# Kernel optimization log

Measured on AMD Instinct MI355X. Metric: run time of the kernel, lower is better.

Reference implementation:

```python
import jax, jax.numpy as jnp
import numpy as np
import math

V, D, H, L, T, B = 32000, 768, 12, 4, 1024, 2
HD = D // H  # head size 64
EMB_SCALE = math.sqrt(D)  # DynamicTanh path
EPS = 1e-5


def setup_inputs() -> dict:
    key = jax.random.key(0)
    ks = jax.random.split(key, 10)
    def rn(k, shape, std=0.02):
        return jax.random.normal(k, shape, jnp.float32) * std
    return {
        "idx": jax.random.randint(ks[0], (B, T), 0, V, dtype=jnp.int32).astype(jnp.int64) if False else jax.random.randint(ks[0], (B, T), 0, V),
        "wte": rn(ks[1], (V, D)),            # tied with lm_head
        "wpe": rn(ks[2], (T, D)),            # block_size == T
        "ln1_alpha": jnp.full((L, 1), 0.5, jnp.float32),
        "ln1_w": jnp.ones((L, D), jnp.float32),
        "ln1_b": jnp.zeros((L, D), jnp.float32),
        "wq": rn(ks[3], (L, D, D)),          # stored [in,out] (torch W.T)
        "wk": rn(ks[4], (L, D, D)),
        "wv": rn(ks[5], (L, D, D)),
        "wo": rn(ks[6], (L, D, D)),
        "bo": jnp.zeros((L, D), jnp.float32),
        "ln2_alpha": jnp.full((L, 1), 0.5, jnp.float32),
        "ln2_w": jnp.ones((L, D), jnp.float32),
        "ln2_b": jnp.zeros((L, D), jnp.float32),
        "w_fc": rn(ks[7], (L, D, 4 * D)),
        "b_fc": jnp.zeros((L, 4 * D), jnp.float32),
        "w_proj": rn(ks[8], (L, 4 * D, D), std=0.02 / math.sqrt(2 * L)),
        "b_proj": jnp.zeros((L, D), jnp.float32),
        "lnf_alpha": jnp.full((1,), 0.5, jnp.float32),
        "lnf_w": jnp.ones((D,), jnp.float32),
        "lnf_b": jnp.zeros((D,), jnp.float32),
    }


def _dyt(x, alpha, w, b):
    # DynamicTanh: layernorm-style normalize, then w * tanh(alpha * xn) + b
    mu = x.mean(-1, keepdims=True)
    var = ((x - mu) ** 2).mean(-1, keepdims=True)
    xn = (x - mu) * jax.lax.rsqrt(var + EPS)
    return w * jnp.tanh(alpha * xn) + b


def reference(idx, wte, wpe, ln1_alpha, ln1_w, ln1_b, wq, wk, wv, wo, bo,
              ln2_alpha, ln2_w, ln2_b, w_fc, b_fc, w_proj, b_proj,
              lnf_alpha, lnf_w, lnf_b):
    Bb, Tt = idx.shape
    x = (wte[idx] + wpe[:Tt][None]) * EMB_SCALE          # [B,T,D]; dropout = eval identity
    mask = jnp.tril(jnp.ones((Tt, Tt), bool))
    scale = 1.0 / math.sqrt(HD)
    for l in range(L):
        h = _dyt(x, ln1_alpha[l], ln1_w[l], ln1_b[l])
        q = (h @ wq[l]).reshape(Bb, Tt, H, HD)
        k = (h @ wk[l]).reshape(Bb, Tt, H, HD)
        v = (h @ wv[l]).reshape(Bb, Tt, H, HD)
        att = jnp.einsum('bqhd,bkhd->bhqk', q, k) * scale
        att = jnp.where(mask, att, -jnp.inf)
        att = jax.nn.softmax(att, axis=-1)
        o = jnp.einsum('bhqk,bkhd->bqhd', att, v).reshape(Bb, Tt, D)
        x = x + o @ wo[l] + bo[l]
        h = _dyt(x, ln2_alpha[l], ln2_w[l], ln2_b[l])
        h = jax.nn.gelu(h @ w_fc[l] + b_fc[l], approximate=False)  # torch nn.GELU = exact erf
        x = x + h @ w_proj[l] + b_proj[l]
    x = _dyt(x, lnf_alpha, lnf_w, lnf_b)
    return x @ wte.T                                     # tied lm_head, [B,T,V]
```

## Files before the change

### kernel.cpp

```cpp
#include <hip/hip_runtime.h>
#include <hip/hip_bf16.h>
#include <math.h>

constexpr int B_ = 2, T_ = 1024, D_ = 768, H_ = 12, L_ = 4, V_ = 32000;
constexpr int M_ = B_ * T_;
constexpr int FF_ = 4 * D_;
constexpr int QKVN_ = 3 * D_;
#define EMB_SCALE 27.712812921102035f
#define EPS_ 1e-5f

typedef __attribute__((ext_vector_type(8))) short short8_t;
typedef __attribute__((ext_vector_type(4))) float float4_t;

__device__ __forceinline__ float bf2f(__hip_bfloat16 v) { return __bfloat162float(v); }
__device__ __forceinline__ __hip_bfloat16 f2bf(float v) { return __float2bfloat16(v); }

__device__ __forceinline__ void gl_lds16(const __hip_bfloat16* g, __hip_bfloat16* l) {
    __builtin_amdgcn_global_load_lds(
        (const __attribute__((address_space(1))) void*)g,
        (__attribute__((address_space(3))) void*)l, 16, 0, 0);
}

__global__ __launch_bounds__(256) void convert_kernel(
    const float* __restrict__ src, __hip_bfloat16* __restrict__ dst, size_t n)
{
    size_t i = ((size_t)blockIdx.x * 256 + threadIdx.x) * 4;
    if (i + 3 < n) {
        float4 f = *(const float4*)(src + i);
        dst[i + 0] = f2bf(f.x);
        dst[i + 1] = f2bf(f.y);
        dst[i + 2] = f2bf(f.z);
        dst[i + 3] = f2bf(f.w);
    }
}

__global__ __launch_bounds__(256) void tconv_kernel(
    const float* __restrict__ src, __hip_bfloat16* __restrict__ dst,
    int K, int N, size_t sstride, size_t dstride)
{
    __shared__ float tile[32][33];
    const float* S = src + (size_t)blockIdx.z * sstride;
    __hip_bfloat16* Dd = dst + (size_t)blockIdx.z * dstride;
    int n0 = blockIdx.x * 32, k0 = blockIdx.y * 32;
    int tx = threadIdx.x & 31, ty = threadIdx.x >> 5;
#pragma unroll
    for (int i = 0; i < 32; i += 8)
        tile[ty + i][tx] = S[(size_t)(k0 + ty + i) * N + n0 + tx];
    __syncthreads();
#pragma unroll
    for (int i = 0; i < 32; i += 8)
        Dd[(size_t)(n0 + ty + i) * K + k0 + tx] = f2bf(tile[tx][ty + i]);
}

__global__ __launch_bounds__(256) void tconv_qkvo_kernel(
    const float* __restrict__ wq, const float* __restrict__ wk,
    const float* __restrict__ wv, const float* __restrict__ wo,
    __hip_bfloat16* __restrict__ wqkv_t, __hip_bfloat16* __restrict__ wo_t)
{
    __shared__ float tile[32][33];
    const int z = blockIdx.z, l = z >> 2, which = z & 3;
    const size_t dd = (size_t)D_ * D_;
    const float* S = (which == 0 ? wq : which == 1 ? wk : which == 2 ? wv : wo) + (size_t)l * dd;
    __hip_bfloat16* Dd = (which < 3) ? wqkv_t + (size_t)l * QKVN_ * D_ + (size_t)which * dd
                                     : wo_t + (size_t)l * dd;
    int n0 = blockIdx.x * 32, k0 = blockIdx.y * 32;
    int tx = threadIdx.x & 31, ty = threadIdx.x >> 5;
#pragma unroll
    for (int i = 0; i < 32; i += 8)
        tile[ty + i][tx] = S[(size_t)(k0 + ty + i) * D_ + n0 + tx];
    __syncthreads();
#pragma unroll
    for (int i = 0; i < 32; i += 8)
        Dd[(size_t)(n0 + ty + i) * D_ + k0 + tx] = f2bf(tile[tx][ty + i]);
}

template <bool EMBED>
__global__ __launch_bounds__(256) void dyt_kernel(
    const float* __restrict__ xin, float* __restrict__ xout,
    __hip_bfloat16* __restrict__ h,
    const float* __restrict__ w, const float* __restrict__ bb,
    const float* __restrict__ alpha_p,
    const int* __restrict__ idx, const float* __restrict__ wte,
    const float* __restrict__ wpe)
{
    const int row = blockIdx.x, tid = threadIdx.x;
    float v[3];
    float s = 0.f, ss = 0.f;
    if (EMBED) {
        const int t = row & (T_ - 1);
        const int tok = idx[row];
#pragma unroll
        for (int i = 0; i < 3; ++i) {
            int c = i * 256 + tid;
            v[i] = (wte[(size_t)tok * D_ + c] + wpe[(size_t)t * D_ + c]) * EMB_SCALE;
            xout[(size_t)row * D_ + c] = v[i];
            s += v[i];
            ss += v[i] * v[i];
        }
    } else {
        const float* xr = xin + (size_t)row * D_;
#pragma unroll
        for (int i = 0; i < 3; ++i) {
            v[i] = xr[i * 256 + tid];
            s += v[i];
            ss += v[i] * v[i];
        }
    }
#pragma unroll
    for (int off = 32; off >= 1; off >>= 1) {
        s  += __shfl_xor(s,  off, 64);
        ss += __shfl_xor(ss, off, 64);
    }
    __shared__ float sh[8];
    int wave = tid >> 6;
    if ((tid & 63) == 0) { sh[wave] = s; sh[wave + 4] = ss; }
    __syncthreads();
    s  = sh[0] + sh[1] + sh[2] + sh[3];
    ss = sh[4] + sh[5] + sh[6] + sh[7];
    float mu = s * (1.f / D_);
    float var = ss * (1.f / D_) - mu * mu;
    float rstd = rsqrtf(var + EPS_);
    float alpha = *alpha_p;
#pragma unroll
    for (int i = 0; i < 3; ++i) {
        int c = i * 256 + tid;
        float xn = (v[i] - mu) * rstd;
        h[(size_t)row * D_ + c] = f2bf(w[c] * tanhf(alpha * xn) + bb[c]);
    }
}

constexpr int LSTR = 72;

__global__ __launch_bounds__(256) void fattn_kernel(
    const __hip_bfloat16* __restrict__ qkv, __hip_bfloat16* __restrict__ o)
{
    const int qt = gridDim.x - 1 - blockIdx.x;
    const int hh = blockIdx.y, b = blockIdx.z;
    const int q0 = qt * 64;
    const int tid = threadIdx.x;
    const int wave = tid >> 6, lane = tid & 63;
    const int quad = lane >> 4, l16 = lane & 15;
    const size_t rs = QKVN_;

    __shared__ __hip_bfloat16 Ks[64 * LSTR];
    __shared__ __hip_bfloat16 Vts[64 * LSTR];
    __shared__ __hip_bfloat16 Ps[4][16 * LSTR];

    const __hip_bfloat16* qrow = qkv + (size_t)(b * T_ + q0 + wave * 16 + l16) * rs + hh * 64;
    short8_t qf0 = *(const short8_t*)(qrow + quad * 8);
    short8_t qf1 = *(const short8_t*)(qrow + 32 + quad * 8);

    float4_t Oacc[4];
#pragma unroll
    for (int j = 0; j < 4; ++j) Oacc[j] = (float4_t){0.f, 0.f, 0.f, 0.f};
    float mrow[4], lrow[4];
#pragma unroll
    for (int r = 0; r < 4; ++r) { mrow[r] = -1e30f; lrow[r] = 0.f; }

    const __hip_bfloat16* kbase = qkv + (size_t)b * T_ * rs + D_ + hh * 64;
    const __hip_bfloat16* vbase = qkv + (size_t)b * T_ * rs + 2 * D_ + hh * 64;

    const int sr = tid >> 2;
    const int sc = (tid & 3) * 8;
    const int vr = lane;
    const int vc0 = wave * 16;

    for (int kt = 0; kt <= qt; ++kt) {
        const int kt0 = kt * 64;
        uint4 kv0 = *(const uint4*)(kbase + (size_t)(kt0 + sr) * rs + sc);
        uint4 kv1 = *(const uint4*)(kbase + (size_t)(kt0 + sr) * rs + sc + 32);
        uint4 vv0 = *(const uint4*)(vbase + (size_t)(kt0 + vr) * rs + vc0);
        uint4 vv1 = *(const uint4*)(vbase + (size_t)(kt0 + vr) * rs + vc0 + 8);
        __syncthreads();
        *(uint4*)(Ks + sr * LSTR + sc)      = kv0;
        *(uint4*)(Ks + sr * LSTR + sc + 32) = kv1;
        {
            const __hip_bfloat16* vp = (const __hip_bfloat16*)&vv0;
#pragma unroll
            for (int i = 0; i < 8; ++i) Vts[(vc0 + i) * LSTR + vr] = vp[i];
            vp = (const __hip_bfloat16*)&vv1;
#pragma unroll
            for (int i = 0; i < 8; ++i) Vts[(vc0 + 8 + i) * LSTR + vr] = vp[i];
        }
        __syncthreads();

        float4_t S[4];
#pragma unroll
        for (int jt = 0; jt < 4; ++jt) {
            short8_t kf0 = *(const short8_t*)(Ks + (jt * 16 + l16) * LSTR + quad * 8);
            short8_t kf1 = *(const short8_t*)(Ks + (jt * 16 + l16) * LSTR + 32 + quad * 8);
            float4_t s = (float4_t){0.f, 0.f, 0.f, 0.f};
            s = __builtin_amdgcn_mfma_f32_16x16x32_bf16(qf0, kf0, s, 0, 0, 0);
            s = __builtin_amdgcn_mfma_f32_16x16x32_bf16(qf1, kf1, s, 0, 0, 0);
            S[jt] = s;
        }

        if (kt == qt) {
#pragma unroll
            for (int jt = 0; jt < 4; ++jt)
#pragma unroll
                for (int r = 0; r < 4; ++r) {
                    int qg = wave * 16 + quad * 4 + r;
                    int kg = jt * 16 + l16;
                    S[jt][r] = (kg > qg) ? -1e30f : S[jt][r] * 0.125f;
                }
        } else {
#pragma unroll
            for (int jt = 0; jt < 4; ++jt)
#pragma unroll
                for (int r = 0; r < 4; ++r) S[jt][r] *= 0.125f;
        }

        float mnew[4], alphav[4];
#pragma unroll
        for (int r = 0; r < 4; ++r) {
            float mx = fmaxf(fmaxf(S[0][r], S[1][r]), fmaxf(S[2][r], S[3][r]));
            mx = fmaxf(mx, __shfl_xor(mx, 1, 64));
            mx = fmaxf(mx, __shfl_xor(mx, 2, 64));
            mx = fmaxf(mx, __shfl_xor(mx, 4, 64));
            mx = fmaxf(mx, __shfl_xor(mx, 8, 64));
            mnew[r] = fmaxf(mrow[r], mx);
            alphav[r] = __expf(mrow[r] - mnew[r]);
            mrow[r] = mnew[r];
        }
        float psum[4] = {0.f, 0.f, 0.f, 0.f};
#pragma unroll
        for (int jt = 0; jt < 4; ++jt)
#pragma unroll
            for (int r = 0; r < 4; ++r) {
                float p = __expf(S[jt][r] - mnew[r]);
                S[jt][r] = p;
                psum[r] += p;
            }
#pragma unroll
        for (int r = 0; r < 4; ++r) {
            float ps = psum[r];
            ps += __shfl_xor(ps, 1, 64);
            ps += __shfl_xor(ps, 2, 64);
            ps += __shfl_xor(ps, 4, 64);
            ps += __shfl_xor(ps, 8, 64);
            lrow[r] = lrow[r] * alphav[r] + ps;
        }

        __hip_bfloat16* ps_base = Ps[wave];
#pragma unroll
        for (int jt = 0; jt < 4; ++jt)
#pragma unroll
            for (int r = 0; r < 4; ++r)
                ps_base[(quad * 4 + r) * LSTR + jt * 16 + l16] = f2bf(S[jt][r]);

#pragma unroll
        for (int j = 0; j < 4; ++j)
#pragma unroll
            for (int r = 0; r < 4; ++r) Oacc[j][r] *= alphav[r];

        short8_t pf0 = *(const short8_t*)(ps_base + l16 * LSTR + quad * 8);
        short8_t pf1 = *(const short8_t*)(ps_base + l16 * LSTR + 32 + quad * 8);
#pragma unroll
        for (int j = 0; j < 4; ++j) {
            short8_t vf0 = *(const short8_t*)(Vts + (j * 16 + l16) * LSTR + quad * 8);
            short8_t vf1 = *(const short8_t*)(Vts + (j * 16 + l16) * LSTR + 32 + quad * 8);
            Oacc[j] = __builtin_amdgcn_mfma_f32_16x16x32_bf16(pf0, vf0, Oacc[j], 0, 0, 0);
            Oacc[j] = __builtin_amdgcn_mfma_f32_16x16x32_bf16(pf1, vf1, Oacc[j], 0, 0, 0);
        }
    }

    float inv_l[4];
#pragma unroll
    for (int r = 0; r < 4; ++r) inv_l[r] = 1.f / lrow[r];
    __hip_bfloat16* orow = o + (size_t)(b * T_ + q0 + wave * 16) * D_ + hh * 64;
#pragma unroll
    for (int j = 0; j < 4; ++j)
#pragma unroll
        for (int r = 0; r < 4; ++r)
            orow[(size_t)(quad * 4 + r) * D_ + j * 16 + l16] = f2bf(Oacc[j][r] * inv_l[r]);
}

__device__ __forceinline__ float gelu_exact(float t) {
    return 0.5f * t * (1.0f + erff(t * 0.70710678118654752f));
}

template <int EPI>
__global__ __launch_bounds__(256, 2) void gemm_btp(
    const __hip_bfloat16* __restrict__ A, const __hip_bfloat16* __restrict__ Bt,
    float* __restrict__ outF, __hip_bfloat16* __restrict__ outB,
    const float* __restrict__ bias, const float* __restrict__ res,
    int M, int N, int K)
{
    __shared__ __hip_bfloat16 lds[4 * 8192];
    const int tid = threadIdx.x;
    const int wave = tid >> 6, lane = tid & 63;
    const int quad = lane >> 4, l16 = lane & 15;
    const int m0 = blockIdx.y * 128, n0 = blockIdx.x * 128;
    const int wm = (wave >> 1) * 64, wn = (wave & 1) * 64;
    const int NT = K >> 5;

    const int srow = tid >> 2;
    const int sq   = (tid & 3) ^ ((srow >> 1) & 3);
    const __hip_bfloat16* gA = A  + (size_t)(m0 + srow) * K + sq * 8;
    const __hip_bfloat16* gB = Bt + (size_t)(n0 + srow) * K + sq * 8;
    char* ldsc = (char*)lds;
    const int wb = wave * 1024;

#define STGP(tt) do {                                                      \
        const size_t ko = (size_t)(tt) * 32;                               \
        char* bb = ldsc + ((tt) & 3) * 16384 + wb;                         \
        gl_lds16(gA + ko,                  (__hip_bfloat16*)(bb));         \
        gl_lds16(gA + (size_t)64 * K + ko, (__hip_bfloat16*)(bb + 4096));  \
        gl_lds16(gB + ko,                  (__hip_bfloat16*)(bb + 8192));  \
        gl_lds16(gB + (size_t)64 * K + ko, (__hip_bfloat16*)(bb + 12288)); \
    } while (0)

    const int xe = (quad ^ ((l16 >> 1) & 3)) * 16;

    float4_t acc[4][4];
#pragma unroll
    for (int i = 0; i < 4; ++i)
#pragma unroll
        for (int j = 0; j < 4; ++j) acc[i][j] = (float4_t){0.f, 0.f, 0.f, 0.f};

    STGP(0); STGP(1); STGP(2);
    asm volatile("s_waitcnt vmcnt(8)" ::: "memory");
    __builtin_amdgcn_sched_barrier(0);
    __builtin_amdgcn_s_barrier();

    for (int t = 0; t < NT; ++t) {
        if (t + 3 < NT) STGP(t + 3);
        const char* base = ldsc + (t & 3) * 16384;
        short8_t af[4], bfv[4];
#pragma unroll
        for (int i = 0; i < 4; ++i)
            af[i]  = *(const short8_t*)(base + (wm + i * 16 + l16) * 64 + xe);
#pragma unroll
        for (int j = 0; j < 4; ++j)
            bfv[j] = *(const short8_t*)(base + 8192 + (wn + j * 16 + l16) * 64 + xe);
        asm volatile("s_waitcnt lgkmcnt(0)" ::: "memory");
        __builtin_amdgcn_sched_barrier(0);
        __builtin_amdgcn_s_setprio(1);
#pragma unroll
        for (int i = 0; i < 4; ++i)
#pragma unroll
            for (int j = 0; j < 4; ++j)
                acc[i][j] = __builtin_amdgcn_mfma_f32_16x16x32_bf16(
                    af[i], bfv[j], acc[i][j], 0, 0, 0);
        __builtin_amdgcn_s_setprio(0);
        if (t + 3 < NT) {
            asm volatile("s_waitcnt vmcnt(8)" ::: "memory");
        } else if (t + 2 < NT) {
            asm volatile("s_waitcnt vmcnt(4)" ::: "memory");
        } else if (t + 1 < NT) {
            asm volatile("s_waitcnt vmcnt(0)" ::: "memory");
        }
        __builtin_amdgcn_sched_barrier(0);
        __builtin_amdgcn_s_barrier();
    }
#undef STGP

#pragma unroll
    for (int i = 0; i < 4; ++i) {
#pragma unroll
        for (int j = 0; j < 4; ++j) {
            int colg = n0 + wn + j * 16 + l16;
#pragma unroll
            for (int rg = 0; rg < 4; ++rg) {
                int rowg = m0 + wm + i * 16 + quad * 4 + rg;
                size_t offo = (size_t)rowg * N + colg;
                float v = acc[i][j][rg];
                if (EPI == 0) {
                    outB[offo] = f2bf(v);
                } else if (EPI == 1) {
                    outF[offo] = res[offo] + v + bias[colg];
                } else if (EPI == 2) {
                    outB[offo] = f2bf(gelu_exact(v + bias[colg]));
                } else {
                    outF[offo] = v;
                }
            }
        }
    }
}

__global__ __launch_bounds__(512, 2) void gemm_lmhead(
    const __hip_bfloat16* __restrict__ A, const __hip_bfloat16* __restrict__ Bt,
    float* __restrict__ out)
{
    constexpr int K = D_;
    constexpr int N = V_;
    constexpr int NT = K / 32;
    __shared__ __hip_bfloat16 lds[4 * 16384];

    const int tid  = threadIdx.x;
    const int wave = tid >> 6, lane = tid & 63;
    const int quad = lane >> 4, l16 = lane & 15;

    const int flat = blockIdx.x;
    const int g = (flat & 7) * 125 + (flat >> 3);
    const int m0 = (g & 7) * 256, n0 = (g >> 3) * 256;

    const int wm = (wave >> 2) * 128;
    const int wn = (wave & 3) * 64;

    const int srow = tid >> 2;
    const int sq   = (tid & 3) ^ ((srow >> 1) & 3);
    const __hip_bfloat16* gA = A  + (size_t)(m0 + srow) * K + sq * 8;
    const __hip_bfloat16* gB = Bt + (size_t)(n0 + srow) * K + sq * 8;
    char* ldsc = (char*)lds;
    const int wb = wave * 1024;

#define STGP(tt) do {                                                        \
        const size_t ko = (size_t)(tt) * 32;                                 \
        char* bb = ldsc + ((tt) & 3) * 32768 + wb;                           \
        gl_lds16(gA + ko,                   (__hip_bfloat16*)(bb));          \
        gl_lds16(gA + (size_t)128 * K + ko, (__hip_bfloat16*)(bb + 8192));   \
        gl_lds16(gB + ko,                   (__hip_bfloat16*)(bb + 16384));  \
        gl_lds16(gB + (size_t)128 * K + ko, (__hip_bfloat16*)(bb + 24576));  \
    } while (0)

    const int xe = (quad ^ ((l16 >> 1) & 3)) * 16;

    float4_t acc[8][4];
#pragma unroll
    for (int i = 0; i < 8; ++i)
#pragma unroll
        for (int j = 0; j < 4; ++j) acc[i][j] = (float4_t){0.f, 0.f, 0.f, 0.f};

    STGP(0); STGP(1); STGP(2);
    asm volatile("s_waitcnt vmcnt(8)" ::: "memory");
    __builtin_amdgcn_sched_barrier(0);
    __builtin_amdgcn_s_barrier();

    for (int t = 0; t < NT; ++t) {
        if (t + 3 < NT) STGP(t + 3);
        const char* base = ldsc + (t & 3) * 32768;
        short8_t af[8], bfv[4];
#pragma unroll
        for (int i = 0; i < 8; ++i)
            af[i]  = *(const short8_t*)(base + (wm + i * 16 + l16) * 64 + xe);
#pragma unroll
        for (int j = 0; j < 4; ++j)
            bfv[j] = *(const short8_t*)(base + 16384 + (wn + j * 16 + l16) * 64 + xe);
        asm volatile("s_waitcnt lgkmcnt(0)" ::: "memory");
        __builtin_amdgcn_sched_barrier(0);
        __builtin_amdgcn_s_setprio(1);
#pragma unroll
        for (int i = 0; i < 8; ++i)
#pragma unroll
            for (int j = 0; j < 4; ++j)
                acc[i][j] = __builtin_amdgcn_mfma_f32_16x16x32_bf16(
                    af[i], bfv[j], acc[i][j], 0, 0, 0);
        __builtin_amdgcn_s_setprio(0);
        if (t + 3 < NT) {
            asm volatile("s_waitcnt vmcnt(8)" ::: "memory");
        } else if (t + 2 < NT) {
            asm volatile("s_waitcnt vmcnt(4)" ::: "memory");
        } else if (t + 1 < NT) {
            asm volatile("s_waitcnt vmcnt(0)" ::: "memory");
        }
        __builtin_amdgcn_sched_barrier(0);
        __builtin_amdgcn_s_barrier();
    }
#undef STGP

    float* orow = out + (size_t)(m0 + wm + quad * 4) * N + (n0 + wn + l16);
#pragma unroll
    for (int i = 0; i < 8; ++i)
#pragma unroll
        for (int j = 0; j < 4; ++j)
#pragma unroll
            for (int rg = 0; rg < 4; ++rg)
                orow[(size_t)(i * 16 + rg) * N + j * 16] = acc[i][j][rg];
}

extern "C" void kernel_launch(void* const* d_in, const int* in_sizes, int n_in,
                              void* d_out, int out_size, void* d_ws, size_t ws_size,
                              hipStream_t stream)
{
    const int*   idx   = (const int*)d_in[0];
    const float* wte   = (const float*)d_in[1];
    const float* wpe   = (const float*)d_in[2];
    const float* ln1_a = (const float*)d_in[3];
    const float* ln1_w = (const float*)d_in[4];
    const float* ln1_b = (const float*)d_in[5];
    const float* wq    = (const float*)d_in[6];
    const float* wk    = (const float*)d_in[7];
    const float* wv    = (const float*)d_in[8];
    const float* wo    = (const float*)d_in[9];
    const float* bo    = (const float*)d_in[10];
    const float* ln2_a = (const float*)d_in[11];
    const float* ln2_w = (const float*)d_in[12];
    const float* ln2_b = (const float*)d_in[13];
    const float* w_fc  = (const float*)d_in[14];
    const float* b_fc  = (const float*)d_in[15];
    const float* w_pr  = (const float*)d_in[16];
    const float* b_pr  = (const float*)d_in[17];
    const float* lnf_a = (const float*)d_in[18];
    const float* lnf_w = (const float*)d_in[19];
    const float* lnf_b = (const float*)d_in[20];
    float* out = (float*)d_out;

    char* ws = (char*)d_ws;
    size_t off = 0;
    auto alloc = [&](size_t bytes) -> char* {
        char* p = ws + off;
        off += (bytes + 255) & ~(size_t)255;
        return p;
    };
    __hip_bfloat16* wqkv_t = (__hip_bfloat16*)alloc((size_t)L_ * QKVN_ * D_ * 2);
    __hip_bfloat16* wo_t   = (__hip_bfloat16*)alloc((size_t)L_ * D_ * D_ * 2);
    __hip_bfloat16* wfc_t  = (__hip_bfloat16*)alloc((size_t)L_ * FF_ * D_ * 2);
    __hip_bfloat16* wpr_t  = (__hip_bfloat16*)alloc((size_t)L_ * D_ * FF_ * 2);
    __hip_bfloat16* wte_b  = (__hip_bfloat16*)alloc((size_t)V_ * D_ * 2);
    float*          x      = (float*)alloc((size_t)M_ * D_ * 4);
    __hip_bfloat16* h      = (__hip_bfloat16*)alloc((size_t)M_ * D_ * 2);
    __hip_bfloat16* qkv    = (__hip_bfloat16*)alloc((size_t)M_ * QKVN_ * 2);
    __hip_bfloat16* attno  = (__hip_bfloat16*)alloc((size_t)M_ * D_ * 2);
    __hip_bfloat16* mid    = (__hip_bfloat16*)alloc((size_t)M_ * FF_ * 2);
    (void)ws_size; (void)in_sizes; (void)n_in; (void)out_size;

    {
        size_t n = (size_t)V_ * D_;
        convert_kernel<<<dim3((unsigned)(n / 1024)), 256, 0, stream>>>(wte, wte_b, n);
    }
    tconv_qkvo_kernel<<<dim3(24, 24, 4 * L_), 256, 0, stream>>>(
        wq, wk, wv, wo, wqkv_t, wo_t);
    tconv_kernel<<<dim3(96, 24, L_), 256, 0, stream>>>(w_fc, wfc_t, D_, FF_, (size_t)D_ * FF_, (size_t)FF_ * D_);
    tconv_kernel<<<dim3(24, 96, L_), 256, 0, stream>>>(w_pr, wpr_t, FF_, D_, (size_t)FF_ * D_, (size_t)D_ * FF_);

    dyt_kernel<true><<<dim3(M_), 256, 0, stream>>>(
        nullptr, x, h, ln1_w, ln1_b, ln1_a, idx, wte, wpe);

    for (int l = 0; l < L_; ++l) {
        if (l > 0)
            dyt_kernel<false><<<dim3(M_), 256, 0, stream>>>(
                x, nullptr, h, ln1_w + l * D_, ln1_b + l * D_, ln1_a + l,
                nullptr, nullptr, nullptr);
        gemm_btp<0><<<dim3(QKVN_ / 128, M_ / 128), 256, 0, stream>>>(
            h, wqkv_t + (size_t)l * QKVN_ * D_, nullptr, qkv, nullptr, nullptr, M_, QKVN_, D_);
        fattn_kernel<<<dim3(T_ / 64, H_, B_), 256, 0, stream>>>(qkv, attno);
        gemm_btp<1><<<dim3(D_ / 128, M_ / 128), 256, 0, stream>>>(
            attno, wo_t + (size_t)l * D_ * D_, x, nullptr, bo + l * D_, x, M_, D_, D_);
        dyt_kernel<false><<<dim3(M_), 256, 0, stream>>>(
            x, nullptr, h, ln2_w + l * D_, ln2_b + l * D_, ln2_a + l,
            nullptr, nullptr, nullptr);
        gemm_btp<2><<<dim3(FF_ / 128, M_ / 128), 256, 0, stream>>>(
            h, wfc_t + (size_t)l * FF_ * D_, nullptr, mid, b_fc + l * FF_, nullptr, M_, FF_, D_);
        gemm_btp<1><<<dim3(D_ / 128, M_ / 128), 256, 0, stream>>>(
            mid, wpr_t + (size_t)l * D_ * FF_, x, nullptr, b_pr + l * D_, x, M_, D_, FF_);
    }

    dyt_kernel<false><<<dim3(M_), 256, 0, stream>>>(
        x, nullptr, h, lnf_w, lnf_b, lnf_a, nullptr, nullptr, nullptr);
    gemm_lmhead<<<dim3((M_ / 256) * (V_ / 256)), 512, 0, stream>>>(h, wte_b, out);
}
```

Measured before the change: 1.114 ms.

## Prefetch next K/V tile in attention and use 64-row GEMM for N=768 projections

In the flash-attention loop, the global loads for the next K/V tile are issued right after the LDS stores, so their latency overlaps the current tile's MFMA and softmax work. A new gemm_btp64 kernel with 64x128 tiles (2x4 accumulators per wave, 4-stage LDS pipeline) replaces the 128x128 GEMM for the output and MLP-projection layers, where N=768. This doubles the block count from 96 to 192 to fill more CUs. The cost is lower arithmetic intensity per block and more register pressure in the attention loop.

```diff
diff --git a/kernel.cpp b/kernel.cpp
--- a/kernel.cpp
+++ b/kernel.cpp
@@ -165,12 +165,12 @@
     const int vr = lane;
     const int vc0 = wave * 16;
 
+    uint4 kv0 = *(const uint4*)(kbase + (size_t)sr * rs + sc);
+    uint4 kv1 = *(const uint4*)(kbase + (size_t)sr * rs + sc + 32);
+    uint4 vv0 = *(const uint4*)(vbase + (size_t)vr * rs + vc0);
+    uint4 vv1 = *(const uint4*)(vbase + (size_t)vr * rs + vc0 + 8);
+
     for (int kt = 0; kt <= qt; ++kt) {
-        const int kt0 = kt * 64;
-        uint4 kv0 = *(const uint4*)(kbase + (size_t)(kt0 + sr) * rs + sc);
-        uint4 kv1 = *(const uint4*)(kbase + (size_t)(kt0 + sr) * rs + sc + 32);
-        uint4 vv0 = *(const uint4*)(vbase + (size_t)(kt0 + vr) * rs + vc0);
-        uint4 vv1 = *(const uint4*)(vbase + (size_t)(kt0 + vr) * rs + vc0 + 8);
         __syncthreads();
         *(uint4*)(Ks + sr * LSTR + sc)      = kv0;
         *(uint4*)(Ks + sr * LSTR + sc + 32) = kv1;
@@ -183,6 +183,14 @@
             for (int i = 0; i < 8; ++i) Vts[(vc0 + 8 + i) * LSTR + vr] = vp[i];
         }
         __syncthreads();
+
+        if (kt < qt) {
+            const int kn0 = (kt + 1) * 64;
+            kv0 = *(const uint4*)(kbase + (size_t)(kn0 + sr) * rs + sc);
+            kv1 = *(const uint4*)(kbase + (size_t)(kn0 + sr) * rs + sc + 32);
+            vv0 = *(const uint4*)(vbase + (size_t)(kn0 + vr) * rs + vc0);
+            vv1 = *(const uint4*)(vbase + (size_t)(kn0 + vr) * rs + vc0 + 8);
+        }
 
         float4_t S[4];
 #pragma unroll
@@ -358,6 +366,105 @@
 
 #pragma unroll
     for (int i = 0; i < 4; ++i) {
+#pragma unroll
+        for (int j = 0; j < 4; ++j) {
+            int colg = n0 + wn + j * 16 + l16;
+#pragma unroll
+            for (int rg = 0; rg < 4; ++rg) {
+                int rowg = m0 + wm + i * 16 + quad * 4 + rg;
+                size_t offo = (size_t)rowg * N + colg;
+                float v = acc[i][j][rg];
+                if (EPI == 0) {
+                    outB[offo] = f2bf(v);
+                } else if (EPI == 1) {
+                    outF[offo] = res[offo] + v + bias[colg];
+                } else if (EPI == 2) {
+                    outB[offo] = f2bf(gelu_exact(v + bias[colg]));
+                } else {
+                    outF[offo] = v;
+                }
+            }
+        }
+    }
+}
+
+template <int EPI>
+__global__ __launch_bounds__(256, 2) void gemm_btp64(
+    const __hip_bfloat16* __restrict__ A, const __hip_bfloat16* __restrict__ Bt,
+    float* __restrict__ outF, __hip_bfloat16* __restrict__ outB,
+    const float* __restrict__ bias, const float* __restrict__ res,
+    int M, int N, int K)
+{
+    __shared__ __hip_bfloat16 lds[4 * 6144];
+    const int tid = threadIdx.x;
+    const int wave = tid >> 6, lane = tid & 63;
+    const int quad = lane >> 4, l16 = lane & 15;
+    const int m0 = blockIdx.y * 64, n0 = blockIdx.x * 128;
+    const int wm = (wave >> 1) * 32, wn = (wave & 1) * 64;
+    const int NT = K >> 5;
+
+    const int srow = tid >> 2;
+    const int sq   = (tid & 3) ^ ((srow >> 1) & 3);
+    const __hip_bfloat16* gA = A  + (size_t)(m0 + srow) * K + sq * 8;
+    const __hip_bfloat16* gB = Bt + (size_t)(n0 + srow) * K + sq * 8;
+    char* ldsc = (char*)lds;
+    const int wb = wave * 1024;
+
+#define STGP64(tt) do {                                                    \
+        const size_t ko = (size_t)(tt) * 32;                               \
+        char* bb = ldsc + ((tt) & 3) * 12288 + wb;                         \
+        gl_lds16(gA + ko,                  (__hip_bfloat16*)(bb));         \
+        gl_lds16(gB + ko,                  (__hip_bfloat16*)(bb + 4096));  \
+        gl_lds16(gB + (size_t)64 * K + ko, (__hip_bfloat16*)(bb + 8192));  \
+    } while (0)
+
+    const int xe = (quad ^ ((l16 >> 1) & 3)) * 16;
+
+    float4_t acc[2][4];
+#pragma unroll
+    for (int i = 0; i < 2; ++i)
+#pragma unroll
+        for (int j = 0; j < 4; ++j) acc[i][j] = (float4_t){0.f, 0.f, 0.f, 0.f};
+
+    STGP64(0); STGP64(1); STGP64(2);
+    asm volatile("s_waitcnt vmcnt(6)" ::: "memory");
+    __builtin_amdgcn_sched_barrier(0);
+    __builtin_amdgcn_s_barrier();
+
+    for (int t = 0; t < NT; ++t) {
+        if (t + 3 < NT) STGP64(t + 3);
+        const char* base = ldsc + (t & 3) * 12288;
+        short8_t af[2], bfv[4];
+#pragma unroll
+        for (int i = 0; i < 2; ++i)
+            af[i]  = *(const short8_t*)(base + (wm + i * 16 + l16) * 64 + xe);
+#pragma unroll
+        for (int j = 0; j < 4; ++j)
+            bfv[j] = *(const short8_t*)(base + 4096 + (wn + j * 16 + l16) * 64 + xe);
+        asm volatile("s_waitcnt lgkmcnt(0)" ::: "memory");
+        __builtin_amdgcn_sched_barrier(0);
+        __builtin_amdgcn_s_setprio(1);
+#pragma unroll
+        for (int i = 0; i < 2; ++i)
+#pragma unroll
+            for (int j = 0; j < 4; ++j)
+                acc[i][j] = __builtin_amdgcn_mfma_f32_16x16x32_bf16(
+                    af[i], bfv[j], acc[i][j], 0, 0, 0);
+        __builtin_amdgcn_s_setprio(0);
+        if (t + 3 < NT) {
+            asm volatile("s_waitcnt vmcnt(6)" ::: "memory");
+        } else if (t + 2 < NT) {
+            asm volatile("s_waitcnt vmcnt(3)" ::: "memory");
+        } else if (t + 1 < NT) {
+            asm volatile("s_waitcnt vmcnt(0)" ::: "memory");
+        }
+        __builtin_amdgcn_sched_barrier(0);
+        __builtin_amdgcn_s_barrier();
+    }
+#undef STGP64
+
+#pragma unroll
+    for (int i = 0; i < 2; ++i) {
 #pragma unroll
         for (int j = 0; j < 4; ++j) {
             int colg = n0 + wn + j * 16 + l16;
@@ -537,14 +644,14 @@
         gemm_btp<0><<<dim3(QKVN_ / 128, M_ / 128), 256, 0, stream>>>(
             h, wqkv_t + (size_t)l * QKVN_ * D_, nullptr, qkv, nullptr, nullptr, M_, QKVN_, D_);
         fattn_kernel<<<dim3(T_ / 64, H_, B_), 256, 0, stream>>>(qkv, attno);
-        gemm_btp<1><<<dim3(D_ / 128, M_ / 128), 256, 0, stream>>>(
+        gemm_btp64<1><<<dim3(D_ / 128, M_ / 64), 256, 0, stream>>>(
             attno, wo_t + (size_t)l * D_ * D_, x, nullptr, bo + l * D_, x, M_, D_, D_);
         dyt_kernel<false><<<dim3(M_), 256, 0, stream>>>(
             x, nullptr, h, ln2_w + l * D_, ln2_b + l * D_, ln2_a + l,
             nullptr, nullptr, nullptr);
         gemm_btp<2><<<dim3(FF_ / 128, M_ / 128), 256, 0, stream>>>(
             h, wfc_t + (size_t)l * FF_ * D_, nullptr, mid, b_fc + l * FF_, nullptr, M_, FF_, D_);
-        gemm_btp<1><<<dim3(D_ / 128, M_ / 128), 256, 0, stream>>>(
+        gemm_btp64<1><<<dim3(D_ / 128, M_ / 64), 256, 0, stream>>>(
             mid, wpr_t + (size_t)l * D_ * FF_, x, nullptr, b_pr + l * D_, x, M_, D_, FF_);
     }
 
```

Result: faster. 1.060 ms (-4.8%).
